# Optimization experiments

Measured on AMD Instinct MI355X. Metric: run time of the kernel, lower is better.

Reference implementation:

```python
import jax, jax.numpy as jnp
import numpy as np

H = 16  # num_attention_heads
LN_EPS = 1e-12


def setup_inputs() -> dict:
    key = jax.random.key(0)
    ks = jax.random.split(key, 13)
    S, B, D = 2048, 2, 1024
    std = 0.02
    return {
        "query_tensor": jax.random.normal(ks[0], (S, B, D), jnp.float32),
        "key_tensor": jax.random.normal(ks[1], (S, B, D), jnp.float32),
        "value_tensor": jax.random.normal(ks[2], (S, B, D), jnp.float32),
        "Wq": jax.random.normal(ks[3], (D, D), jnp.float32) * std,
        "bq": jnp.zeros((D,), jnp.float32),
        "Wk": jax.random.normal(ks[4], (D, D), jnp.float32) * std,
        "bk": jnp.zeros((D,), jnp.float32),
        "Wv": jax.random.normal(ks[5], (D, D), jnp.float32) * std,
        "bv": jnp.zeros((D,), jnp.float32),
        "Wo": jax.random.normal(ks[6], (D, D), jnp.float32) * std,
        "bo": jnp.zeros((D,), jnp.float32),
        "ln_w": jnp.ones((D,), jnp.float32),
        "ln_b": jnp.zeros((D,), jnp.float32),
    }


def _layernorm(x, w, b):
    u = jnp.mean(x, axis=-1, keepdims=True)
    s = jnp.mean(jnp.square(x - u), axis=-1, keepdims=True)
    return w * ((x - u) / jnp.sqrt(s + LN_EPS)) + b


def reference(query_tensor, key_tensor, value_tensor, Wq, bq, Wk, bk, Wv, bv, Wo, bo, ln_w, ln_b):
    S, B, D = query_tensor.shape
    dh = D // H
    # QKV projections (nn.Linear: x @ W.T + b)
    q = query_tensor @ Wq.T + bq          # (S, B, D)
    k = key_tensor @ Wk.T + bk            # (Sk, B, D)
    v = value_tensor @ Wv.T + bv          # (Sk, B, D)
    # (S, B, D) -> (B*H, S, dh)
    q = q.reshape(S, B * H, dh).transpose(1, 0, 2)
    k = k.reshape(-1, B * H, dh).transpose(1, 0, 2)
    v = v.reshape(-1, B * H, dh).transpose(1, 0, 2)
    # NOTE: original code has NO 1/sqrt(dh) scaling
    scores = jnp.einsum('nqd,nkd->nqk', q, k)            # (B*H, S, Sk)
    probs = jax.nn.softmax(scores, axis=-1)
    # dropout is identity in eval mode
    ctx = jnp.einsum('nqk,nkd->nqd', probs, v)           # (B*H, S, dh)
    ctx = ctx.transpose(1, 0, 2).reshape(S, B, D)
    # BertSelfOutput: dense + residual + LayerNorm (dropout identity)
    out = ctx @ Wo.T + bo
    return _layernorm(out + query_tensor, ln_w, ln_b)
```

## Files before the change

### kernel.cpp

```cpp
#include <hip/hip_runtime.h>

#define SEQ    2048
#define BATCH  2
#define DMODEL 1024
#define NHEAD  16
#define DH     64
#define MROWS  (SEQ*BATCH)
#define RS     (BATCH*DMODEL)
#define LN_EPS 1e-12f

typedef __attribute__((ext_vector_type(8))) short short8;
typedef __attribute__((ext_vector_type(4))) float floatx4;

#define AS_GLOBAL __attribute__((address_space(1)))
#define AS_LDS    __attribute__((address_space(3)))

__device__ __forceinline__ float bf2f(unsigned short s) {
    union { unsigned u; float f; } a; a.u = ((unsigned)s) << 16; return a.f;
}
__device__ __forceinline__ unsigned short f2bf(float x) {
    union { float f; unsigned u; } a; a.f = x;
    unsigned r = a.u + 0x7fffu + ((a.u >> 16) & 1u);
    return (unsigned short)(r >> 16);
}
__device__ __forceinline__ uint4 cvt8(const float* __restrict__ p) {
    float4 x0 = *(const float4*)(p);
    float4 x1 = *(const float4*)(p + 4);
    union { uint4 u; unsigned short s[8]; } r;
    r.s[0] = f2bf(x0.x); r.s[1] = f2bf(x0.y);
    r.s[2] = f2bf(x0.z); r.s[3] = f2bf(x0.w);
    r.s[4] = f2bf(x1.x); r.s[5] = f2bf(x1.y);
    r.s[6] = f2bf(x1.z); r.s[7] = f2bf(x1.w);
    return r.u;
}

__global__ void beacon_kernel(float* out, float val) {
    if (threadIdx.x == 0) out[0] = val;
}

__global__ __launch_bounds__(256)
void cvt_kernel(const float* __restrict__ s0, const float* __restrict__ s1,
                const float* __restrict__ s2, const float* __restrict__ s3,
                const float* __restrict__ s4, const float* __restrict__ s5,
                const float* __restrict__ s6,
                unsigned short* __restrict__ d0, unsigned short* __restrict__ d1,
                unsigned short* __restrict__ d2, unsigned short* __restrict__ d3,
                unsigned short* __restrict__ d4, unsigned short* __restrict__ d5,
                unsigned short* __restrict__ d6)
{
    const float* srcs[7] = {s0, s1, s2, s3, s4, s5, s6};
    unsigned short* dsts[7] = {d0, d1, d2, d3, d4, d5, d6};
    const int cnts[7] = {4194304, 4194304, 4194304, 1048576, 1048576, 1048576, 1048576};
    const int z = blockIdx.z;
    const float* src = srcs[z];
    unsigned short* dst = dsts[z];
    const int count = cnts[z];
    const int stride = gridDim.x * 256 * 8;
    for (int i = (blockIdx.x * 256 + threadIdx.x) * 8; i < count; i += stride)
        *(uint4*)&dst[i] = cvt8(&src[i]);
}

template<int OUTF32>
__device__ __forceinline__ void gemm_bf16_body(
    const unsigned short* __restrict__ A,
    const unsigned short* __restrict__ W,
    const float* __restrict__ bias,
    void* __restrict__ Cout)
{
    __shared__ __align__(16) short Alds[128*32];
    __shared__ __align__(16) short Blds[128*32];

    const int tid  = threadIdx.x;
    const int lane = tid & 63;
    const int wave = tid >> 6;
    const int lrow = lane & 15;
    const int lq   = lane >> 4;
    const int m0 = blockIdx.x * 128;
    const int n0 = blockIdx.y * 128;
    const int mw = (wave >> 1) * 64;
    const int nw = (wave & 1) * 64;
    const int K  = DMODEL;

    const int chunk0 = tid;
    const int chunk1 = tid + 256;
    const int row0 = chunk0 >> 2, col0 = (chunk0 & 3) << 3;
    const int row1 = chunk1 >> 2, col1 = (chunk1 & 3) << 3;
    const unsigned short* gA0 = &A[(m0 + row0) * K + col0];
    const unsigned short* gA1 = &A[(m0 + row1) * K + col1];
    const unsigned short* gB0 = &W[(n0 + row0) * K + col0];
    const unsigned short* gB1 = &W[(n0 + row1) * K + col1];
    AS_LDS unsigned int* lA0 = (AS_LDS unsigned int*)&Alds[(wave*64)*8];
    AS_LDS unsigned int* lA1 = (AS_LDS unsigned int*)&Alds[(256 + wave*64)*8];
    AS_LDS unsigned int* lB0 = (AS_LDS unsigned int*)&Blds[(wave*64)*8];
    AS_LDS unsigned int* lB1 = (AS_LDS unsigned int*)&Blds[(256 + wave*64)*8];

    floatx4 zero = {0.f, 0.f, 0.f, 0.f};
    floatx4 acc[4][4];
    #pragma unroll
    for (int i = 0; i < 4; ++i)
        #pragma unroll
        for (int j = 0; j < 4; ++j) acc[i][j] = zero;

    for (int k0 = 0; k0 < K; k0 += 32) {
        __builtin_amdgcn_global_load_lds((const AS_GLOBAL unsigned int*)(gA0 + k0), lA0, 16, 0, 0);
        __builtin_amdgcn_global_load_lds((const AS_GLOBAL unsigned int*)(gA1 + k0), lA1, 16, 0, 0);
        __builtin_amdgcn_global_load_lds((const AS_GLOBAL unsigned int*)(gB0 + k0), lB0, 16, 0, 0);
        __builtin_amdgcn_global_load_lds((const AS_GLOBAL unsigned int*)(gB1 + k0), lB1, 16, 0, 0);
        __syncthreads();
        short8 af[4], bfg[4];
        #pragma unroll
        for (int mi = 0; mi < 4; ++mi)
            af[mi] = *(const short8*)&Alds[(mw + mi*16 + lrow)*32 + lq*8];
        #pragma unroll
        for (int ni = 0; ni < 4; ++ni)
            bfg[ni] = *(const short8*)&Blds[(nw + ni*16 + lrow)*32 + lq*8];
        #pragma unroll
        for (int mi = 0; mi < 4; ++mi)
            #pragma unroll
            for (int ni = 0; ni < 4; ++ni)
                acc[mi][ni] = __builtin_amdgcn_mfma_f32_16x16x32_bf16(af[mi], bfg[ni], acc[mi][ni], 0, 0, 0);
        __syncthreads();
    }

    #pragma unroll
    for (int mi = 0; mi < 4; ++mi) {
        #pragma unroll
        for (int ni = 0; ni < 4; ++ni) {
            int n = n0 + nw + ni*16 + lrow;
            float bv_ = bias[n];
            #pragma unroll
            for (int r = 0; r < 4; ++r) {
                int m = m0 + mw + mi*16 + lq*4 + r;
                float v = acc[mi][ni][r] + bv_;
                if (OUTF32) ((float*)Cout)[m * DMODEL + n] = v;
                else ((unsigned short*)Cout)[m * DMODEL + n] = f2bf(v);
            }
        }
    }
}

__global__ __launch_bounds__(256)
void qkv_bf16(const unsigned short* __restrict__ qb, const unsigned short* __restrict__ kb,
              const unsigned short* __restrict__ vb,
              const unsigned short* __restrict__ Wqb, const float* __restrict__ bq,
              const unsigned short* __restrict__ Wkb, const float* __restrict__ bk,
              const unsigned short* __restrict__ Wvb, const float* __restrict__ bv,
              unsigned short* __restrict__ Qo, unsigned short* __restrict__ Ko,
              unsigned short* __restrict__ Vo)
{
    const unsigned short *A, *W; const float* B; unsigned short* C;
    if (blockIdx.z == 0)      { A = qb; W = Wqb; B = bq; C = Qo; }
    else if (blockIdx.z == 1) { A = kb; W = Wkb; B = bk; C = Ko; }
    else                      { A = vb; W = Wvb; B = bv; C = Vo; }
    gemm_bf16_body<0>(A, W, B, C);
}

__global__ __launch_bounds__(256)
void oproj_bf16(const unsigned short* __restrict__ Cx,
                const unsigned short* __restrict__ Wob, const float* __restrict__ bo,
                float* __restrict__ O32)
{
    gemm_bf16_body<1>(Cx, Wob, bo, O32);
}

__global__ __launch_bounds__(256)
void qkv_mfma(const float* __restrict__ q_in, const float* __restrict__ k_in,
              const float* __restrict__ v_in,
              const float* __restrict__ Wq, const float* __restrict__ bq,
              const float* __restrict__ Wk, const float* __restrict__ bk,
              const float* __restrict__ Wv, const float* __restrict__ bv,
              unsigned short* __restrict__ Qo, unsigned short* __restrict__ Ko,
              unsigned short* __restrict__ Vo)
{
    const float *A, *W, *B; unsigned short* C;
    if (blockIdx.z == 0)      { A = q_in; W = Wq; B = bq; C = Qo; }
    else if (blockIdx.z == 1) { A = k_in; W = Wk; B = bk; C = Ko; }
    else                      { A = v_in; W = Wv; B = bv; C = Vo; }

    __shared__ __align__(16) short Alds[128*32];
    __shared__ __align__(16) short Blds[128*32];
    const int tid  = threadIdx.x;
    const int lane = tid & 63;
    const int wave = tid >> 6;
    const int lrow = lane & 15;
    const int lq   = lane >> 4;
    const int m0 = blockIdx.x * 128;
    const int n0 = blockIdx.y * 128;
    const int mw = (wave >> 1) * 64;
    const int nw = (wave & 1) * 64;
    const int K  = DMODEL;

    floatx4 zero = {0.f, 0.f, 0.f, 0.f};
    floatx4 acc[4][4];
    #pragma unroll
    for (int i = 0; i < 4; ++i)
        #pragma unroll
        for (int j = 0; j < 4; ++j) acc[i][j] = zero;

    for (int k0 = 0; k0 < K; k0 += 32) {
        #pragma unroll
        for (int rep = 0; rep < 2; ++rep) {
            int chunk = tid + rep * 256;
            int row = chunk >> 2;
            int col = (chunk & 3) << 3;
            *(uint4*)&Alds[row*32 + col] = cvt8(&A[(m0 + row) * K + k0 + col]);
            *(uint4*)&Blds[row*32 + col] = cvt8(&W[(n0 + row) * K + k0 + col]);
        }
        __syncthreads();
        short8 af[4], bfg[4];
        #pragma unroll
        for (int mi = 0; mi < 4; ++mi)
            af[mi] = *(const short8*)&Alds[(mw + mi*16 + lrow)*32 + lq*8];
        #pragma unroll
        for (int ni = 0; ni < 4; ++ni)
            bfg[ni] = *(const short8*)&Blds[(nw + ni*16 + lrow)*32 + lq*8];
        #pragma unroll
        for (int mi = 0; mi < 4; ++mi)
            #pragma unroll
            for (int ni = 0; ni < 4; ++ni)
                acc[mi][ni] = __builtin_amdgcn_mfma_f32_16x16x32_bf16(af[mi], bfg[ni], acc[mi][ni], 0, 0, 0);
        __syncthreads();
    }

    #pragma unroll
    for (int mi = 0; mi < 4; ++mi) {
        #pragma unroll
        for (int ni = 0; ni < 4; ++ni) {
            int n = n0 + nw + ni*16 + lrow;
            float bv_ = B[n];
            #pragma unroll
            for (int r = 0; r < 4; ++r) {
                int m = m0 + mw + mi*16 + lq*4 + r;
                C[m * DMODEL + n] = f2bf(acc[mi][ni][r] + bv_);
            }
        }
    }
}

__global__ __launch_bounds__(256)
void oproj_mfma(const unsigned short* __restrict__ Cx,
                const float* __restrict__ Wo, const float* __restrict__ bo,
                float* __restrict__ O32)
{
    __shared__ __align__(16) short Alds[128*32];
    __shared__ __align__(16) short Blds[128*32];
    const int tid  = threadIdx.x;
    const int lane = tid & 63;
    const int wave = tid >> 6;
    const int lrow = lane & 15;
    const int lq   = lane >> 4;
    const int m0 = blockIdx.x * 128;
    const int n0 = blockIdx.y * 128;
    const int mw = (wave >> 1) * 64;
    const int nw = (wave & 1) * 64;
    const int K  = DMODEL;

    floatx4 zero = {0.f, 0.f, 0.f, 0.f};
    floatx4 acc[4][4];
    #pragma unroll
    for (int i = 0; i < 4; ++i)
        #pragma unroll
        for (int j = 0; j < 4; ++j) acc[i][j] = zero;

    for (int k0 = 0; k0 < K; k0 += 32) {
        #pragma unroll
        for (int rep = 0; rep < 2; ++rep) {
            int chunk = tid + rep * 256;
            int row = chunk >> 2;
            int col = (chunk & 3) << 3;
            *(uint4*)&Alds[row*32 + col] = *(const uint4*)&Cx[(m0 + row) * K + k0 + col];
            *(uint4*)&Blds[row*32 + col] = cvt8(&Wo[(n0 + row) * K + k0 + col]);
        }
        __syncthreads();
        short8 af[4], bfg[4];
        #pragma unroll
        for (int mi = 0; mi < 4; ++mi)
            af[mi] = *(const short8*)&Alds[(mw + mi*16 + lrow)*32 + lq*8];
        #pragma unroll
        for (int ni = 0; ni < 4; ++ni)
            bfg[ni] = *(const short8*)&Blds[(nw + ni*16 + lrow)*32 + lq*8];
        #pragma unroll
        for (int mi = 0; mi < 4; ++mi)
            #pragma unroll
            for (int ni = 0; ni < 4; ++ni)
                acc[mi][ni] = __builtin_amdgcn_mfma_f32_16x16x32_bf16(af[mi], bfg[ni], acc[mi][ni], 0, 0, 0);
        __syncthreads();
    }

    #pragma unroll
    for (int mi = 0; mi < 4; ++mi) {
        #pragma unroll
        for (int ni = 0; ni < 4; ++ni) {
            int n = n0 + nw + ni*16 + lrow;
            float bv_ = bo[n];
            #pragma unroll
            for (int r = 0; r < 4; ++r) {
                int m = m0 + mw + mi*16 + lq*4 + r;
                O32[m * DMODEL + n] = acc[mi][ni][r] + bv_;
            }
        }
    }
}

__global__ __launch_bounds__(256)
void attn_mfma2(const unsigned short* __restrict__ Q,
                const unsigned short* __restrict__ Kg,
                const unsigned short* __restrict__ V,
                unsigned short* __restrict__ Ctx)
{
    __shared__ __align__(16) short Qs[64*72];
    __shared__ __align__(16) short Ks[64*72];
    __shared__ __align__(16) short Vt[64*72];
    __shared__ __align__(16) short Ps[4][16*72];

    const int tid  = threadIdx.x;
    const int lane = tid & 63;
    const int wave = tid >> 6;
    const int lrow = lane & 15;
    const int lq   = lane >> 4;

    const int q0 = blockIdx.x * 64;
    const int bh = blockIdx.y;
    const int off = (bh >> 4) * DMODEL + (bh & 15) * DH;

    #pragma unroll
    for (int rep = 0; rep < 2; ++rep) {
        int chunk = tid + rep * 256;
        int r = chunk >> 3;
        int c = (chunk & 7) << 3;
        *(uint4*)&Qs[r*72 + c] = *(const uint4*)&Q[(q0 + r) * RS + off + c];
    }
    __syncthreads();

    short8 qf[2];
    #pragma unroll
    for (int ks = 0; ks < 2; ++ks)
        qf[ks] = *(const short8*)&Qs[(wave*16 + lrow)*72 + ks*32 + lq*8];

    floatx4 zero = {0.f, 0.f, 0.f, 0.f};
    float m_i = -1e30f, l_i = 0.f;
    floatx4 oacc[4];
    #pragma unroll
    for (int ni = 0; ni < 4; ++ni) oacc[ni] = zero;

    for (int kt = 0; kt < SEQ/64; ++kt) {
        __syncthreads();
        const int kbase = kt * 64;
        #pragma unroll
        for (int rep = 0; rep < 2; ++rep) {
            int chunk = tid + rep * 256;
            int r = chunk >> 3;
            int c = (chunk & 7) << 3;
            *(uint4*)&Ks[r*72 + c] = *(const uint4*)&Kg[(kbase + r) * RS + off + c];
            uint4 vv = *(const uint4*)&V[(kbase + r) * RS + off + c];
            union { uint4 u; short s[8]; } uv; uv.u = vv;
            int swz = (chunk & 7) << 3;
            #pragma unroll
            for (int j = 0; j < 8; ++j)
                Vt[(c + j)*72 + (r ^ swz)] = uv.s[j];
        }
        __syncthreads();

        floatx4 sacc[4];
        #pragma unroll
        for (int ni = 0; ni < 4; ++ni) sacc[ni] = zero;
        #pragma unroll
        for (int ni = 0; ni < 4; ++ni) {
            #pragma unroll
            for (int ks = 0; ks < 2; ++ks) {
                short8 kf = *(const short8*)&Ks[(ni*16 + lrow)*72 + ks*32 + lq*8];
                sacc[ni] = __builtin_amdgcn_mfma_f32_16x16x32_bf16(kf, qf[ks], sacc[ni], 0, 0, 0);
            }
        }

        float mx = sacc[0][0];
        #pragma unroll
        for (int ni = 0; ni < 4; ++ni)
            #pragma unroll
            for (int r = 0; r < 4; ++r) mx = fmaxf(mx, sacc[ni][r]);
        mx = fmaxf(mx, __shfl_xor(mx, 16));
        mx = fmaxf(mx, __shfl_xor(mx, 32));
        float mnew = fmaxf(m_i, mx);
        float alpha = __expf(m_i - mnew);
        float p[4][4];
        float psum = 0.f;
        #pragma unroll
        for (int ni = 0; ni < 4; ++ni)
            #pragma unroll
            for (int r = 0; r < 4; ++r) {
                p[ni][r] = __expf(sacc[ni][r] - mnew);
                psum += p[ni][r];
            }
        psum += __shfl_xor(psum, 16);
        psum += __shfl_xor(psum, 32);
        l_i = l_i * alpha + psum;
        m_i = mnew;
        #pragma unroll
        for (int ni = 0; ni < 4; ++ni)
            #pragma unroll
            for (int r = 0; r < 4; ++r) oacc[ni][r] *= alpha;

        #pragma unroll
        for (int ni = 0; ni < 4; ++ni) {
            uint2 pk;
            pk.x = (unsigned)f2bf(p[ni][0]) | ((unsigned)f2bf(p[ni][1]) << 16);
            pk.y = (unsigned)f2bf(p[ni][2]) | ((unsigned)f2bf(p[ni][3]) << 16);
            *(uint2*)&Ps[wave][lrow*72 + ni*16 + lq*4] = pk;
        }
        __builtin_amdgcn_wave_barrier();

        short8 pf[2];
        #pragma unroll
        for (int ks = 0; ks < 2; ++ks)
            pf[ks] = *(const short8*)&Ps[wave][lrow*72 + ks*32 + lq*8];
        #pragma unroll
        for (int ni = 0; ni < 4; ++ni) {
            #pragma unroll
            for (int ks = 0; ks < 2; ++ks) {
                int d  = ni*16 + lrow;
                int kk = ks*32 + lq*8;
                int swz = ((d >> 3) & 7) << 3;
                short8 vf = *(const short8*)&Vt[d*72 + (kk ^ swz)];
                oacc[ni] = __builtin_amdgcn_mfma_f32_16x16x32_bf16(vf, pf[ks], oacc[ni], 0, 0, 0);
            }
        }
    }

    const float inv = 1.f / l_i;
    const int q = q0 + wave*16 + lrow;
    #pragma unroll
    for (int ni = 0; ni < 4; ++ni) {
        uint2 ok;
        ok.x = (unsigned)f2bf(oacc[ni][0] * inv) | ((unsigned)f2bf(oacc[ni][1] * inv) << 16);
        ok.y = (unsigned)f2bf(oacc[ni][2] * inv) | ((unsigned)f2bf(oacc[ni][3] * inv) << 16);
        *(uint2*)&Ctx[q * RS + off + ni*16 + lq*4] = ok;
    }
}

__global__ __launch_bounds__(256)
void ln2_kernel(const float* __restrict__ O,
                const float* __restrict__ resid,
                const float* __restrict__ w,
                const float* __restrict__ bb,
                float* __restrict__ out)
{
    __shared__ float r1[256];
    __shared__ float r2[256];
    const int row = blockIdx.x;
    const int tid = threadIdx.x;
    const int c4 = tid * 4;

    float4 o4 = *(const float4*)&O[row * DMODEL + c4];
    float4 q4 = *(const float4*)&resid[row * DMODEL + c4];
    float x0 = o4.x + q4.x;
    float x1 = o4.y + q4.y;
    float x2 = o4.z + q4.z;
    float x3 = o4.w + q4.w;

    r1[tid] = x0 + x1 + x2 + x3;
    r2[tid] = x0*x0 + x1*x1 + x2*x2 + x3*x3;
    __syncthreads();
    for (int st = 128; st > 0; st >>= 1) {
        if (tid < st) { r1[tid] += r1[tid + st]; r2[tid] += r2[tid + st]; }
        __syncthreads();
    }
    const float mean = r1[0] * (1.f / DMODEL);
    float var = r2[0] * (1.f / DMODEL) - mean * mean;
    var = fmaxf(var, 0.f);
    const float rstd = rsqrtf(var + LN_EPS);

    float4 w4 = *(const float4*)&w[c4];
    float4 b4 = *(const float4*)&bb[c4];
    float4 y;
    y.x = w4.x * ((x0 - mean) * rstd) + b4.x;
    y.y = w4.y * ((x1 - mean) * rstd) + b4.y;
    y.z = w4.z * ((x2 - mean) * rstd) + b4.z;
    y.w = w4.w * ((x3 - mean) * rstd) + b4.w;
    *(float4*)&out[row * DMODEL + c4] = y;
}

extern "C" void kernel_launch(void* const* d_in, const int* in_sizes, int n_in,
                              void* d_out, int out_size, void* d_ws, size_t ws_size,
                              hipStream_t stream) {
    const float* q_in = (const float*)d_in[0];
    const float* k_in = (const float*)d_in[1];
    const float* v_in = (const float*)d_in[2];
    const float* Wq = (const float*)d_in[3];  const float* bq = (const float*)d_in[4];
    const float* Wk = (const float*)d_in[5];  const float* bk = (const float*)d_in[6];
    const float* Wv = (const float*)d_in[7];  const float* bv = (const float*)d_in[8];
    const float* Wo = (const float*)d_in[9];  const float* bo = (const float*)d_in[10];
    const float* lnw = (const float*)d_in[11]; const float* lnb = (const float*)d_in[12];

    char* wsb = (char*)d_ws;
    unsigned short* QCtx = (unsigned short*)d_out;
    float*          outF = (float*)d_out;
    dim3 blk(256);

    if (ws_size >= (48u << 20)) {
        unsigned short* qb  = (unsigned short*)(wsb);
        unsigned short* kb  = (unsigned short*)(wsb + (8u  << 20));
        unsigned short* vb  = (unsigned short*)(wsb + (16u << 20));
        unsigned short* Wqb = (unsigned short*)(wsb + (24u << 20));
        unsigned short* Wkb = (unsigned short*)(wsb + (26u << 20));
        unsigned short* Wvb = (unsigned short*)(wsb + (28u << 20));
        unsigned short* Wob = (unsigned short*)(wsb + (30u << 20));
        unsigned short* Kb  = (unsigned short*)(wsb + (32u << 20));
        unsigned short* Vb  = (unsigned short*)(wsb + (40u << 20));
        float*          O32 = (float*)(wsb);

        cvt_kernel<<<dim3(512, 1, 7), blk, 0, stream>>>(
            q_in, k_in, v_in, Wq, Wk, Wv, Wo,
            qb, kb, vb, Wqb, Wkb, Wvb, Wob);
        qkv_bf16<<<dim3(MROWS/128, DMODEL/128, 3), blk, 0, stream>>>(
            qb, kb, vb, Wqb, bq, Wkb, bk, Wvb, bv, QCtx, Kb, Vb);
        attn_mfma2<<<dim3(SEQ/64, BATCH*NHEAD), blk, 0, stream>>>(QCtx, Kb, Vb, QCtx);
        oproj_bf16<<<dim3(MROWS/128, DMODEL/128), blk, 0, stream>>>(QCtx, Wob, bo, O32);
        ln2_kernel<<<dim3(MROWS), blk, 0, stream>>>(O32, q_in, lnw, lnb, outF);
    } else if (ws_size >= (16u << 20)) {
        unsigned short* Kb  = (unsigned short*)(wsb);
        unsigned short* Vb  = (unsigned short*)(wsb + (8u << 20));
        float*          O32 = (float*)(wsb);
        qkv_mfma<<<dim3(MROWS/128, DMODEL/128, 3), blk, 0, stream>>>(
            q_in, k_in, v_in, Wq, bq, Wk, bk, Wv, bv, QCtx, Kb, Vb);
        attn_mfma2<<<dim3(SEQ/64, BATCH*NHEAD), blk, 0, stream>>>(QCtx, Kb, Vb, QCtx);
        oproj_mfma<<<dim3(MROWS/128, DMODEL/128), blk, 0, stream>>>(QCtx, Wo, bo, O32);
        ln2_kernel<<<dim3(MROWS), blk, 0, stream>>>(O32, q_in, lnw, lnb, outF);
    } else {
        beacon_kernel<<<1, 64, 0, stream>>>((float*)d_out, 300.0f);
    }
}
```

Measured before the change: 273.7 us.

## Pre-transpose V and stream K/V tiles into LDS with direct swizzled loads

Adds a separate kernel that transposes V into a per-head (d, seq) layout, so the attention kernel can read V^T tiles contiguously. The new attention kernel fills Q, K and V^T tiles in LDS with global_load_lds DMA using an XOR swizzle in place of padded rows, which removes the register round-trip and the in-kernel transpose. In exchange it adds one extra launch and one extra read and write of V, and it reuses the workspace region holding the bf16 query copy, which is assumed dead by then.

```diff
diff --git a/kernel.cpp b/kernel.cpp
--- a/kernel.cpp
+++ b/kernel.cpp
@@ -58,6 +58,36 @@
     const int stride = gridDim.x * 256 * 8;
     for (int i = (blockIdx.x * 256 + threadIdx.x) * 8; i < count; i += stride)
         *(uint4*)&dst[i] = cvt8(&src[i]);
+}
+
+__global__ __launch_bounds__(256)
+void vt_kernel(const unsigned short* __restrict__ Vb,
+               unsigned short* __restrict__ VT)
+{
+    __shared__ __align__(16) short T[64*72];
+    const int tid = threadIdx.x;
+    const int s0 = blockIdx.x * 64;
+    const int bh = blockIdx.y;
+    const int b = bh >> 4, h = bh & 15;
+
+    #pragma unroll
+    for (int rep = 0; rep < 2; ++rep) {
+        int c = tid + rep * 256;
+        int s = c >> 3, cc = c & 7;
+        *(uint4*)&T[s*72 + cc*8] =
+            *(const uint4*)&Vb[((s0 + s) * BATCH + b) * DMODEL + h*64 + cc*8];
+    }
+    __syncthreads();
+    #pragma unroll
+    for (int rep = 0; rep < 2; ++rep) {
+        int o = tid + rep * 256;
+        int d = o >> 3, sc = o & 7;
+        union { uint4 u; unsigned short e[8]; } pk;
+        #pragma unroll
+        for (int j = 0; j < 8; ++j)
+            pk.e[j] = (unsigned short)T[(sc*8 + j)*72 + d];
+        *(uint4*)&VT[bh*(DH*SEQ) + d*SEQ + s0 + sc*8] = pk.u;
+    }
 }
 
 template<int OUTF32>
@@ -303,6 +333,146 @@
 }
 
 __global__ __launch_bounds__(256)
+void attn_mfma3(const unsigned short* __restrict__ Q,
+                const unsigned short* __restrict__ Kg,
+                const unsigned short* __restrict__ VT,
+                unsigned short* __restrict__ Ctx)
+{
+    __shared__ __align__(16) short Qs[64*64];
+    __shared__ __align__(16) short Ks[64*64];
+    __shared__ __align__(16) short Vt[64*64];
+    __shared__ __align__(16) short Ps[4][16*72];
+
+    const int tid  = threadIdx.x;
+    const int lane = tid & 63;
+    const int wave = tid >> 6;
+    const int lrow = lane & 15;
+    const int lq   = lane >> 4;
+
+    const int q0 = blockIdx.x * 64;
+    const int bh = blockIdx.y;
+    const int off = (bh >> 4) * DMODEL + (bh & 15) * DH;
+    const unsigned short* VTb = VT + bh * (DH * SEQ);
+
+    #pragma unroll
+    for (int rep = 0; rep < 2; ++rep) {
+        int c = rep*256 + wave*64 + lane;
+        int r = c >> 3, cc = c & 7;
+        const unsigned short* g = &Q[(q0 + r) * RS + off + ((cc ^ (r & 7)) << 3)];
+        AS_LDS unsigned int* l = (AS_LDS unsigned int*)&Qs[(rep*256 + wave*64) * 8];
+        __builtin_amdgcn_global_load_lds((const AS_GLOBAL unsigned int*)g, l, 16, 0, 0);
+    }
+    __syncthreads();
+
+    short8 qf[2];
+    #pragma unroll
+    for (int ks = 0; ks < 2; ++ks) {
+        int r = wave*16 + lrow;
+        int cc = ks*4 + lq;
+        qf[ks] = *(const short8*)&Qs[r*64 + ((cc ^ (r & 7)) << 3)];
+    }
+
+    floatx4 zero = {0.f, 0.f, 0.f, 0.f};
+    float m_i = -1e30f, l_i = 0.f;
+    floatx4 oacc[4];
+    #pragma unroll
+    for (int ni = 0; ni < 4; ++ni) oacc[ni] = zero;
+
+    for (int kt = 0; kt < SEQ/64; ++kt) {
+        __syncthreads();
+        const int kbase = kt * 64;
+        #pragma unroll
+        for (int rep = 0; rep < 2; ++rep) {
+            int c = rep*256 + wave*64 + lane;
+            int r = c >> 3, cc = c & 7;
+            int sw = ((cc ^ (r & 7)) << 3);
+            const unsigned short* gk = &Kg[(kbase + r) * RS + off + sw];
+            const unsigned short* gv = &VTb[r * SEQ + kbase + sw];
+            AS_LDS unsigned int* lk = (AS_LDS unsigned int*)&Ks[(rep*256 + wave*64) * 8];
+            AS_LDS unsigned int* lv = (AS_LDS unsigned int*)&Vt[(rep*256 + wave*64) * 8];
+            __builtin_amdgcn_global_load_lds((const AS_GLOBAL unsigned int*)gk, lk, 16, 0, 0);
+            __builtin_amdgcn_global_load_lds((const AS_GLOBAL unsigned int*)gv, lv, 16, 0, 0);
+        }
+        __syncthreads();
+
+        floatx4 sacc[4];
+        #pragma unroll
+        for (int ni = 0; ni < 4; ++ni) sacc[ni] = zero;
+        #pragma unroll
+        for (int ni = 0; ni < 4; ++ni) {
+            #pragma unroll
+            for (int ks = 0; ks < 2; ++ks) {
+                int key = ni*16 + lrow;
+                int cc  = ks*4 + lq;
+                short8 kf = *(const short8*)&Ks[key*64 + ((cc ^ (key & 7)) << 3)];
+                sacc[ni] = __builtin_amdgcn_mfma_f32_16x16x32_bf16(kf, qf[ks], sacc[ni], 0, 0, 0);
+            }
+        }
+
+        float mx = sacc[0][0];
+        #pragma unroll
+        for (int ni = 0; ni < 4; ++ni)
+            #pragma unroll
+            for (int r = 0; r < 4; ++r) mx = fmaxf(mx, sacc[ni][r]);
+        mx = fmaxf(mx, __shfl_xor(mx, 16));
+        mx = fmaxf(mx, __shfl_xor(mx, 32));
+        float mnew = fmaxf(m_i, mx);
+        float alpha = __expf(m_i - mnew);
+        float p[4][4];
+        float psum = 0.f;
+        #pragma unroll
+        for (int ni = 0; ni < 4; ++ni)
+            #pragma unroll
+            for (int r = 0; r < 4; ++r) {
+                p[ni][r] = __expf(sacc[ni][r] - mnew);
+                psum += p[ni][r];
+            }
+        psum += __shfl_xor(psum, 16);
+        psum += __shfl_xor(psum, 32);
+        l_i = l_i * alpha + psum;
+        m_i = mnew;
+        #pragma unroll
+        for (int ni = 0; ni < 4; ++ni)
+            #pragma unroll
+            for (int r = 0; r < 4; ++r) oacc[ni][r] *= alpha;
+
+        #pragma unroll
+        for (int ni = 0; ni < 4; ++ni) {
+            uint2 pk;
+            pk.x = (unsigned)f2bf(p[ni][0]) | ((unsigned)f2bf(p[ni][1]) << 16);
+            pk.y = (unsigned)f2bf(p[ni][2]) | ((unsigned)f2bf(p[ni][3]) << 16);
+            *(uint2*)&Ps[wave][lrow*72 + ni*16 + lq*4] = pk;
+        }
+        __builtin_amdgcn_wave_barrier();
+
+        short8 pf[2];
+        #pragma unroll
+        for (int ks = 0; ks < 2; ++ks)
+            pf[ks] = *(const short8*)&Ps[wave][lrow*72 + ks*32 + lq*8];
+        #pragma unroll
+        for (int ni = 0; ni < 4; ++ni) {
+            #pragma unroll
+            for (int ks = 0; ks < 2; ++ks) {
+                int d  = ni*16 + lrow;
+                int cc = ks*4 + lq;
+                short8 vf = *(const short8*)&Vt[d*64 + ((cc ^ (d & 7)) << 3)];
+                oacc[ni] = __builtin_amdgcn_mfma_f32_16x16x32_bf16(vf, pf[ks], oacc[ni], 0, 0, 0);
+            }
+        }
+    }
+
+    const float inv = 1.f / l_i;
+    const int q = q0 + wave*16 + lrow;
+    #pragma unroll
+    for (int ni = 0; ni < 4; ++ni) {
+        uint2 ok;
+        ok.x = (unsigned)f2bf(oacc[ni][0] * inv) | ((unsigned)f2bf(oacc[ni][1] * inv) << 16);
+        ok.y = (unsigned)f2bf(oacc[ni][2] * inv) | ((unsigned)f2bf(oacc[ni][3] * inv) << 16);
+        *(uint2*)&Ctx[q * RS + off + ni*16 + lq*4] = ok;
+    }
+}
+
+__global__ __launch_bounds__(256)
 void attn_mfma2(const unsigned short* __restrict__ Q,
                 const unsigned short* __restrict__ Kg,
                 const unsigned short* __restrict__ V,
@@ -506,6 +676,7 @@
         unsigned short* Wob = (unsigned short*)(wsb + (30u << 20));
         unsigned short* Kb  = (unsigned short*)(wsb + (32u << 20));
         unsigned short* Vb  = (unsigned short*)(wsb + (40u << 20));
+        unsigned short* VT  = (unsigned short*)(wsb);
         float*          O32 = (float*)(wsb);
 
         cvt_kernel<<<dim3(512, 1, 7), blk, 0, stream>>>(
@@ -513,7 +684,8 @@
             qb, kb, vb, Wqb, Wkb, Wvb, Wob);
         qkv_bf16<<<dim3(MROWS/128, DMODEL/128, 3), blk, 0, stream>>>(
             qb, kb, vb, Wqb, bq, Wkb, bk, Wvb, bv, QCtx, Kb, Vb);
-        attn_mfma2<<<dim3(SEQ/64, BATCH*NHEAD), blk, 0, stream>>>(QCtx, Kb, Vb, QCtx);
+        vt_kernel<<<dim3(SEQ/64, BATCH*NHEAD), blk, 0, stream>>>(Vb, VT);
+        attn_mfma3<<<dim3(SEQ/64, BATCH*NHEAD), blk, 0, stream>>>(QCtx, Kb, VT, QCtx);
         oproj_bf16<<<dim3(MROWS/128, DMODEL/128), blk, 0, stream>>>(QCtx, Wob, bo, O32);
         ln2_kernel<<<dim3(MROWS), blk, 0, stream>>>(O32, q_in, lnw, lnb, outF);
     } else if (ws_size >= (16u << 20)) {
```

Measured after the change: 270.2 us. No clear change (-1.3%).
